# Optimization experiments

Hardware: AMD Instinct MI355X
Metric: run time of the kernel (lower is better)

Reference implementation:

```python
import jax, jax.numpy as jnp
import numpy as np

N_STATE = 64
N_LAYERS = 4
D_MODEL = 512
D_OUT = 256
BATCH = 16
SEQLEN = 2048


def setup_inputs() -> dict:
    key = jax.random.key(0)
    ks = jax.random.split(key, 16)
    H, N, nl = D_MODEL, N_STATE, N_LAYERS
    inp = {}
    inp["x"] = jax.random.normal(ks[0], (BATCH, SEQLEN, D_MODEL), dtype=jnp.float32)
    # encoder / decoder dense
    inp["enc_w"] = jax.random.normal(ks[1], (D_MODEL, D_MODEL), jnp.float32) / np.sqrt(D_MODEL)
    inp["enc_b"] = jnp.zeros((D_MODEL,), jnp.float32)
    inp["dec_w"] = jax.random.normal(ks[2], (D_MODEL, D_OUT), jnp.float32) / np.sqrt(D_MODEL)
    inp["dec_b"] = jnp.zeros((D_OUT,), jnp.float32)
    # per-layer LayerNorm
    inp["ln_scale"] = jnp.ones((nl, D_MODEL), jnp.float32)
    inp["ln_bias"] = jnp.zeros((nl, D_MODEL), jnp.float32)
    # per-layer S4 DPLR params (stored as real/imag float pairs)
    inp["lambda_re"] = -0.5 * jnp.ones((nl, H, N), jnp.float32)
    inp["lambda_im"] = jnp.broadcast_to(np.pi * jnp.arange(N, dtype=jnp.float32), (nl, H, N))
    inp["p_re"] = jax.random.normal(ks[3], (nl, H, N), jnp.float32) * 0.5
    inp["p_im"] = jax.random.normal(ks[4], (nl, H, N), jnp.float32) * 0.5
    inp["b_re"] = jax.random.normal(ks[5], (nl, H, N), jnp.float32) * 0.5
    inp["b_im"] = jax.random.normal(ks[6], (nl, H, N), jnp.float32) * 0.5
    inp["c_re"] = jax.random.normal(ks[7], (nl, H, N), jnp.float32) * 0.5
    inp["c_im"] = jax.random.normal(ks[8], (nl, H, N), jnp.float32) * 0.5
    inp["log_step"] = jax.random.uniform(ks[9], (nl, H), jnp.float32, minval=np.log(1e-3), maxval=np.log(1e-1))
    inp["d_param"] = jnp.ones((nl, H), jnp.float32)
    # per-layer output Dense
    inp["out_w"] = jax.random.normal(ks[10], (nl, D_MODEL, D_MODEL), jnp.float32) / np.sqrt(D_MODEL)
    inp["out_b"] = jnp.zeros((nl, D_MODEL), jnp.float32)
    return inp


def _layer_norm(x, scale, bias, eps=1e-6):
    mu = jnp.mean(x, axis=-1, keepdims=True)
    var = jnp.mean(jnp.square(x - mu), axis=-1, keepdims=True)
    return (x - mu) * jax.lax.rsqrt(var + eps) * scale + bias


def _kernel_dplr(Lam, P, B, C, step, L):
    # Lam,P,B,C: [H,N] complex64; step: [H] float32 -> K: [H,L] float32
    theta = (2.0 * np.pi / L) * jnp.arange(L, dtype=jnp.float32)
    Omega = jnp.exp(-1j * theta)                        # [L] roots of unity
    g = (2.0 / step)[:, None] * ((1.0 - Omega) / (1.0 + Omega))[None, :]  # [H,L]
    c = 2.0 / (1.0 + Omega)                             # [L]
    r = 1.0 / (g[:, :, None] - Lam[:, None, :])         # [H,L,N] resolvent (Cauchy)
    Cc, Pc = jnp.conj(C), jnp.conj(P)
    k00 = jnp.einsum("hn,hln->hl", Cc * B, r)
    k01 = jnp.einsum("hn,hln->hl", Cc * P, r)
    k10 = jnp.einsum("hn,hln->hl", Pc * B, r)
    k11 = jnp.einsum("hn,hln->hl", Pc * P, r)
    at_roots = c[None, :] * (k00 - k01 * (1.0 / (1.0 + k11)) * k10)  # [H,L]
    return jnp.fft.ifft(at_roots, n=L, axis=-1).real


def _s4_apply(u, Lam, P, B, C, step, D):
    # u: [Bt,L,H]; causal FFT convolution with kernel K[h,:] per channel
    L = u.shape[1]
    K = _kernel_dplr(Lam, P, B, C, step, L)             # [H,L]
    ud = jnp.fft.rfft(u, n=2 * L, axis=1)               # [Bt,L+1,H]
    Kd = jnp.fft.rfft(K, n=2 * L, axis=-1)              # [H,L+1]
    y = jnp.fft.irfft(ud * Kd.T[None], n=2 * L, axis=1)[:, :L]
    return y + D[None, None, :] * u


def reference(x, enc_w, enc_b, ln_scale, ln_bias, lambda_re, lambda_im,
              p_re, p_im, b_re, b_im, c_re, c_im, log_step, d_param,
              out_w, out_b, dec_w, dec_b):
    h = x @ enc_w + enc_b
    n_layers = ln_scale.shape[0]
    for i in range(n_layers):
        skip = h
        z = _layer_norm(h, ln_scale[i], ln_bias[i])
        Lam = lambda_re[i] + 1j * lambda_im[i]
        P = p_re[i] + 1j * p_im[i]
        B = b_re[i] + 1j * b_im[i]
        C = c_re[i] + 1j * c_im[i]
        z = _s4_apply(z, Lam, P, B, C, jnp.exp(log_step[i]), d_param[i])
        z = jax.nn.gelu(z)
        z = z @ out_w[i] + out_b[i]
        h = skip + z  # dropout=0.0 -> identity
    logits = h @ dec_w + dec_b
    return jax.nn.log_softmax(logits, axis=-1)
```

## Files before the change

kernel.cpp:

```cpp
#include <hip/hip_runtime.h>
#include <hip/hip_bf16.h>

#define NLAY 4
#define DH   512
#define NST  64
#define NB   16
#define SL   2048
#define NDO  256
#define BL   (NB*SL)
#define KDIM 512
#define TWOPI 6.283185307179586476925287

typedef unsigned short u16;
typedef __attribute__((ext_vector_type(8))) short  short8v;
typedef __attribute__((ext_vector_type(8))) unsigned short ushort8v;
typedef __attribute__((ext_vector_type(4))) float  f32x4;
typedef __attribute__((ext_vector_type(2))) unsigned int uint2v;

#define RCPF(x) __builtin_amdgcn_rcpf(x)

__device__ __forceinline__ float bf2f(u16 v){
  union { unsigned u; float f; } x; x.u = ((unsigned)v) << 16; return x.f;
}
__device__ __forceinline__ u16 f2bf(float f){
  union { float f; unsigned u; } x; x.f = f;
  unsigned u = x.u;
  unsigned r = u + 0x7fffu + ((u >> 16) & 1u);
  return (u16)(r >> 16);
}
__device__ __forceinline__ void cmulw(float& xr, float& xi, float wr, float wi){
  float tr = xr*wr - xi*wi;
  xi = fmaf(xr, wi, xi*wr);
  xr = tr;
}
__device__ __forceinline__ float gelu_fast(float v){
  const float c0 = 0.7978845608028654f;
  float u = c0 * fmaf(0.044715f, v*v*v, v);
  return v * RCPF(1.0f + __expf(-2.0f * u));
}
__device__ __forceinline__ void gload16(const void* g, void* l){
  __builtin_amdgcn_global_load_lds(
      (__attribute__((address_space(1))) void*)(g),
      (__attribute__((address_space(3))) void*)(l), 16, 0, 0);
}

__device__ __forceinline__ void twapply(float* re, float* im, float a){
  float ci, cr;
  __sincosf(a, &ci, &cr);
  float wr = cr, wi = ci;
#pragma unroll
  for (int k = 1; k < 16; k++){
    cmulw(re[k], im[k], wr, wi);
    const float nr = wr*cr - wi*ci;
    wi = fmaf(wr, ci, wi*cr);
    wr = nr;
  }
}

template<int SGN>
__device__ __forceinline__ void dft4w(float& r0, float& i0, float& r1, float& i1,
                                      float& r2, float& i2, float& r3, float& i3){
  const float t0r = r0 + r2, t0i = i0 + i2;
  const float t1r = r0 - r2, t1i = i0 - i2;
  const float t2r = r1 + r3, t2i = i1 + i3;
  const float t3r = r1 - r3, t3i = i1 - i3;
  r0 = t0r + t2r; i0 = t0i + t2i;
  r2 = t0r - t2r; i2 = t0i - t2i;
  if (SGN < 0){ r1 = t1r + t3i; i1 = t1i - t3r; r3 = t1r - t3i; i3 = t1i + t3r; }
  else        { r1 = t1r - t3i; i1 = t1i + t3r; r3 = t1r + t3i; i3 = t1i - t3r; }
}

template<int SGN>
__device__ __forceinline__ void dft16tail(float* re, float* im){
  const float C1 = 0.92387953251128675613f, S1_ = 0.38268343236508977172f;
  const float C2 = 0.70710678118654752440f;
  const float sg = (SGN < 0) ? -1.f : 1.f;
  cmulw(re[5],  im[5],   C1,  sg*S1_);
  cmulw(re[9],  im[9],   C2,  sg*C2);
  cmulw(re[13], im[13],  S1_, sg*C1);
  cmulw(re[6],  im[6],   C2,  sg*C2);
  cmulw(re[10], im[10],  0.f, sg*1.f);
  cmulw(re[14], im[14], -C2,  sg*C2);
  cmulw(re[7],  im[7],   S1_, sg*C1);
  cmulw(re[11], im[11], -C2,  sg*C2);
  cmulw(re[15], im[15], -C1,  sg*(-S1_));
#pragma unroll
  for (int c = 0; c < 4; c++)
    dft4w<SGN>(re[4*c], im[4*c], re[4*c+1], im[4*c+1], re[4*c+2], im[4*c+2], re[4*c+3], im[4*c+3]);
  float tr_, ti_;
#define SWP(A,B) tr_=re[A]; re[A]=re[B]; re[B]=tr_; ti_=im[A]; im[A]=im[B]; im[B]=ti_;
  SWP(1,4) SWP(2,8) SWP(3,12) SWP(6,9) SWP(7,13) SWP(11,14)
#undef SWP
}

template<int SGN>
__device__ __forceinline__ void dft16(float* re, float* im){
#pragma unroll
  for (int b = 0; b < 4; b++)
    dft4w<SGN>(re[b], im[b], re[4+b], im[4+b], re[8+b], im[8+b], re[12+b], im[12+b]);
  dft16tail<SGN>(re, im);
}

__device__ __forceinline__ void dft16fh(float* re, float* im){
#pragma unroll
  for (int b = 0; b < 4; b++){
    const float r0 = re[b], i0 = im[b], r1 = re[4+b], i1 = im[4+b];
    re[b]    = r0 + r1; im[b]    = i0 + i1;
    re[4+b]  = r0 + i1; im[4+b]  = i0 - r1;
    re[8+b]  = r0 - r1; im[8+b]  = i0 - i1;
    re[12+b] = r0 - i1; im[12+b] = i0 + r1;
  }
  dft16tail<-1>(re, im);
}

__device__ __forceinline__ int cxpad(int i){ return i + (i >> 4) + ((i >> 8) << 1); }
#define CXSZ 4384

__device__ __forceinline__ void fwd4096(float* re, float* im, float2* cx, int t){
  dft16fh(re, im);
  twapply(re, im, -(float)(TWOPI/4096.0) * (float)t);
#pragma unroll
  for (int k = 0; k < 16; k++) cx[cxpad(t + 256*k)] = make_float2(re[k], im[k]);
  __syncthreads();
  const int k1 = t >> 4, m2 = t & 15;
  const int b2 = k1*256 + m2;
#pragma unroll
  for (int j = 0; j < 16; j++){ float2 v = cx[cxpad(b2 + 16*j)]; re[j] = v.x; im[j] = v.y; }
  dft16<-1>(re, im);
  twapply(re, im, -(float)(TWOPI/256.0) * (float)m2);
#pragma unroll
  for (int k = 0; k < 16; k++) cx[cxpad(b2 + 16*k)] = make_float2(re[k], im[k]);
  __syncthreads();
#pragma unroll
  for (int j = 0; j < 16; j++){ float2 v = cx[cxpad(16*t + j)]; re[j] = v.x; im[j] = v.y; }
  dft16<-1>(re, im);
}

__device__ __forceinline__ void inv4096(float* re, float* im, float2* cx, int t){
  dft16<1>(re, im);
#pragma unroll
  for (int j = 0; j < 16; j++) cx[cxpad(16*t + j)] = make_float2(re[j], im[j]);
  __syncthreads();
  const int k1 = t >> 4, m2 = t & 15;
  const int b2 = k1*256 + m2;
#pragma unroll
  for (int k = 0; k < 16; k++){ float2 v = cx[cxpad(b2 + 16*k)]; re[k] = v.x; im[k] = v.y; }
  twapply(re, im, (float)(TWOPI/256.0) * (float)m2);
  dft16<1>(re, im);
#pragma unroll
  for (int j = 0; j < 16; j++) cx[cxpad(b2 + 16*j)] = make_float2(re[j], im[j]);
  __syncthreads();
#pragma unroll
  for (int k = 0; k < 16; k++){ float2 v = cx[cxpad(t + 256*k)]; re[k] = v.x; im[k] = v.y; }
  twapply(re, im, (float)(TWOPI/4096.0) * (float)t);
  dft16<1>(re, im);
}

__global__ __launch_bounds__(256) void prep_k(
  const float* __restrict__ lam_re, const float* __restrict__ lam_im,
  const float* __restrict__ p_re,  const float* __restrict__ p_im,
  const float* __restrict__ b_re,  const float* __restrict__ b_im,
  const float* __restrict__ c_re,  const float* __restrict__ c_im,
  float4* __restrict__ cwA, float4* __restrict__ cwB, float* __restrict__ cwS)
{
  const int i = blockIdx.x * 256 + threadIdx.x;
  const float lr = lam_re[i], li = lam_im[i];
  const float pr = p_re[i],  pi = p_im[i];
  const float br = b_re[i],  bi = b_im[i];
  const float cr = c_re[i],  ci = c_im[i];
  cwA[i] = make_float4(lr, li, cr*br + ci*bi, cr*bi - ci*br);
  cwB[i] = make_float4(cr*pr + ci*pi, cr*pi - ci*pr, pr*br + pi*bi, pr*bi - pi*br);
  cwS[i] = pr*pr + pi*pi;
}

__global__ __launch_bounds__(256) void cauchy_k(
    const float4* __restrict__ cwA, const float4* __restrict__ cwB,
    const float* __restrict__ cwS, const float* __restrict__ lstep,
    float2* __restrict__ Kd)
{
  const int t = threadIdx.x;
  const int h = blockIdx.y, lay = blockIdx.z;
  const int lb = blockIdx.x * 256 + t;
  const int wb = (lay*DH + h) * NST;
  const float tw0 = 2.0f * expf(-lstep[lay*DH + h]);

  float T0,T1, g0,g1;
  { float sn, cs;
    sincosf((float)(TWOPI/4096.0)*(float)(lb       ), &sn, &cs); T0 = sn*RCPF(cs); g0 = tw0*T0;
    sincosf((float)(TWOPI/4096.0)*(float)(lb + 1024), &sn, &cs); T1 = sn*RCPF(cs); g1 = tw0*T1;
  }

  float k00r0=0,k00i0=0,k01r0=0,k01i0=0,k10r0=0,k10i0=0,k11r0=0,k11i0=0;
  float k00r1=0,k00i1=0,k01r1=0,k01i1=0,k10r1=0,k10i1=0,k11r1=0,k11i1=0;

#pragma unroll 2
  for (int n = 0; n < NST; n++){
    const float4 A  = cwA[wb + n];
    const float4 Bv = cwB[wb + n];
    const float w11 = cwS[wb + n];
    const float nlr = -A.x;
    const float dr2 = A.x * A.x;
#define CSTEP(J) { \
    const float di = g##J - A.y; \
    const float sI = RCPF(fmaf(di, di, dr2)); \
    const float ivr = nlr * sI, ivi = -di * sI; \
    k00r##J = fmaf(A.z,  ivr, fmaf(-A.w,  ivi, k00r##J)); \
    k00i##J = fmaf(A.z,  ivi, fmaf( A.w,  ivr, k00i##J)); \
    k01r##J = fmaf(Bv.x, ivr, fmaf(-Bv.y, ivi, k01r##J)); \
    k01i##J = fmaf(Bv.x, ivi, fmaf( Bv.y, ivr, k01i##J)); \
    k10r##J = fmaf(Bv.z, ivr, fmaf(-Bv.w, ivi, k10r##J)); \
    k10i##J = fmaf(Bv.z, ivi, fmaf( Bv.w, ivr, k10i##J)); \
    k11r##J = fmaf(w11,  ivr, k11r##J); \
    k11i##J = fmaf(w11,  ivi, k11i##J); }
    CSTEP(0) CSTEP(1)
#undef CSTEP
  }

  float2* kp = Kd + (size_t)(lay*DH + h) * 4096;
#define COUT(J, LOFF) { \
    const float d1r = 1.f + k11r##J, d1i = k11i##J; \
    const float idn = RCPF(fmaf(d1r, d1r, d1i*d1i)); \
    const float wr = k01r##J*k10r##J - k01i##J*k10i##J; \
    const float wi = k01r##J*k10i##J + k01i##J*k10r##J; \
    const float vr = fmaf(wr, d1r,  wi*d1i) * idn; \
    const float vi = fmaf(wi, d1r, -wr*d1i) * idn; \
    const float sr = k00r##J - vr, si = k00i##J - vi; \
    kp[lb + LOFF] = make_float2(fmaf(-T##J, si, sr), fmaf(T##J, sr, si)); }
  COUT(0, 0) COUT(1, 1024)
#undef COUT
}

__global__ __launch_bounds__(256) void kdfft_k(float2* __restrict__ Kd){
  __shared__ float  ar[SL], ai[SL];
  __shared__ float2 cx[CXSZ];
  const int t = threadIdx.x;
  const size_t base = (size_t)blockIdx.x * 4096;
#pragma unroll
  for (int q = 0; q < 8; q++){
    const int l = t + 256*q;
    float2 v = Kd[base + l];
    const int brv = __brev((unsigned)l) >> 21;
    ar[brv] = v.x; ai[brv] = v.y;
  }
  __syncthreads();

  for (int s = 0; s < 11; s++){
    const int half = 1 << s;
    const float fac = (float)(TWOPI) / (float)(2 << s);
#pragma unroll
    for (int q = 0; q < 4; q++){
      const int v = t + 256*q;
      const int pos = v & (half - 1);
      const int i0 = ((v >> s) << (s+1)) + pos;
      const int i1 = i0 + half;
      const float ang = fac * (float)pos;
      const float wc = __cosf(ang), ws = __sinf(ang);
      const float xr = ar[i1], xi = ai[i1];
      const float tr = wc*xr - ws*xi, ti = fmaf(wc, xi, ws*xr);
      const float ur_ = ar[i0], ui_ = ai[i0];
      ar[i0] = ur_ + tr; ai[i0] = ui_ + ti;
      ar[i1] = ur_ - tr; ai[i1] = ui_ - ti;
    }
    __syncthreads();
  }

  float re[16], im[16];
#pragma unroll
  for (int j = 0; j < 16; j++){
    re[j] = (j < 8) ? ar[t + 256*j] * (1.0f/2048.f) : 0.f;
    im[j] = 0.f;
  }
  fwd4096(re, im, cx, t);
  float2* kp = Kd + base + 16*t;
#pragma unroll
  for (int k = 0; k < 16; k += 2)
    *(float4*)(kp + k) = make_float4(re[k], im[k], re[k+1], im[k+1]);
}

__global__ __launch_bounds__(256) void wconv_all_k(
    const float* __restrict__ enc_w, const float* __restrict__ out_w,
    const float* __restrict__ dec_w, u16* __restrict__ Wt)
{
  const int z = blockIdx.z;
  const float* src; u16* dst; int N;
  if (z == 0){ src = enc_w; dst = Wt; N = DH; }
  else if (z <= 4){ src = out_w + (size_t)(z-1)*KDIM*DH; dst = Wt + (size_t)z*262144; N = DH; }
  else { if (blockIdx.y >= 4) return; src = dec_w; dst = Wt + (size_t)5*262144; N = NDO; }
  __shared__ u16 tile[64][72];
  const int k0 = blockIdx.x * 64, n0 = blockIdx.y * 64;
  const int r = threadIdx.x >> 2, c4 = (threadIdx.x & 3) * 16;
  const float* s = src + (size_t)(k0 + r) * N + n0 + c4;
  float4 f0 = *(const float4*)s, f1 = *(const float4*)(s+4);
  float4 f2 = *(const float4*)(s+8), f3 = *(const float4*)(s+12);
  tile[c4+0][r]=f2bf(f0.x); tile[c4+1][r]=f2bf(f0.y); tile[c4+2][r]=f2bf(f0.z); tile[c4+3][r]=f2bf(f0.w);
  tile[c4+4][r]=f2bf(f1.x); tile[c4+5][r]=f2bf(f1.y); tile[c4+6][r]=f2bf(f1.z); tile[c4+7][r]=f2bf(f1.w);
  tile[c4+8][r]=f2bf(f2.x); tile[c4+9][r]=f2bf(f2.y); tile[c4+10][r]=f2bf(f2.z); tile[c4+11][r]=f2bf(f2.w);
  tile[c4+12][r]=f2bf(f3.x); tile[c4+13][r]=f2bf(f3.y); tile[c4+14][r]=f2bf(f3.z); tile[c4+15][r]=f2bf(f3.w);
  __syncthreads();
  u16* d = dst + (size_t)(n0 + r) * KDIM + k0 + c4;
  *(ushort8v*)d       = *(const ushort8v*)&tile[r][c4];
  *(ushort8v*)(d + 8) = *(const ushort8v*)&tile[r][c4 + 8];
}

#define LTILE 32
__device__ __forceinline__ int lnswz(int h){ return ((h >> 1) + (h >> 6)) & 3; }

__global__ __launch_bounds__(256) void lnt_k(const u16* __restrict__ hsrc,
    const float* __restrict__ gam, const float* __restrict__ bet,
    u16* __restrict__ zT){
  __shared__ u16 tile[DH][LTILE];
  __shared__ float smu[LTILE], srs[LTILE];
  const int t = threadIdx.x;
  const int b = blockIdx.y, l0 = blockIdx.x * LTILE;
  const int r = t >> 3, hb = (t & 7) * 64;
  const u16* p = hsrc + ((size_t)b * SL + l0 + r) * DH + hb;
  float s = 0.f, sq = 0.f;
#pragma unroll
  for (int j8 = 0; j8 < 8; j8++){
    ushort8v w = *(const ushort8v*)(p + j8*8);
    const int h0 = hb + j8*8;
#pragma unroll
    for (int d = 0; d < 8; d++){
      const float f = bf2f((u16)w[d]);
      s += f; sq = fmaf(f, f, sq);
      tile[h0+d][r ^ (lnswz(h0+d) << 3)] = (u16)w[d];
    }
  }
  s  += __shfl_xor(s, 1);  sq += __shfl_xor(sq, 1);
  s  += __shfl_xor(s, 2);  sq += __shfl_xor(sq, 2);
  s  += __shfl_xor(s, 4);  sq += __shfl_xor(sq, 4);
  if ((t & 7) == 0){
    const float mu = s * (1.0f/DH);
    smu[r] = mu;
    srs[r] = rsqrtf(sq * (1.0f/DH) - mu*mu + 1e-6f);
  }
  __syncthreads();

#pragma unroll
  for (int hh = 0; hh < 2; hh++){
    const int h = t + hh*256;
    const float g = gam[h], be = bet[h];
    const int sw = lnswz(h);
    u16* dst = zT + ((size_t)b * DH + h) * SL + l0;
#pragma unroll
    for (int og = 0; og < 4; og++){
      const int lg = og ^ sw;
      ushort8v v = *(const ushort8v*)&tile[h][og*8];
      const float4 m0 = *(const float4*)&smu[lg*8];
      const float4 m1 = *(const float4*)&smu[lg*8 + 4];
      const float4 r0 = *(const float4*)&srs[lg*8];
      const float4 r1 = *(const float4*)&srs[lg*8 + 4];
      ushort8v o;
      o[0] = f2bf(fmaf(bf2f((u16)v[0]) - m0.x, r0.x*g, be));
      o[1] = f2bf(fmaf(bf2f((u16)v[1]) - m0.y, r0.y*g, be));
      o[2] = f2bf(fmaf(bf2f((u16)v[2]) - m0.z, r0.z*g, be));
      o[3] = f2bf(fmaf(bf2f((u16)v[3]) - m0.w, r0.w*g, be));
      o[4] = f2bf(fmaf(bf2f((u16)v[4]) - m1.x, r1.x*g, be));
      o[5] = f2bf(fmaf(bf2f((u16)v[5]) - m1.y, r1.y*g, be));
      o[6] = f2bf(fmaf(bf2f((u16)v[6]) - m1.z, r1.z*g, be));
      o[7] = f2bf(fmaf(bf2f((u16)v[7]) - m1.w, r1.w*g, be));
      *(ushort8v*)(dst + lg*8) = o;
    }
  }
}

__global__ __launch_bounds__(256) void s4conv_k(
    const u16* __restrict__ zT, const float2* __restrict__ Kd,
    const float* __restrict__ dpar, u16* __restrict__ yT)
{
  __shared__ float2 cx[CXSZ];
  const int t = threadIdx.x;
  const int wg = blockIdx.x;
  const int h = wg & 511, bp = wg >> 9;
  const u16* r1 = zT + ((size_t)(2*bp) * DH + h) * SL;
  const u16* r2 = r1 + (size_t)DH * SL;
  float ur1[8], ur2[8];
  float re[16], im[16];
#pragma unroll
  for (int j = 0; j < 8; j++){
    ur1[j] = bf2f(r1[t + 256*j]);
    ur2[j] = bf2f(r2[t + 256*j]);
    re[j] = ur1[j]; im[j] = ur2[j];
  }
#pragma unroll
  for (int j = 8; j < 16; j++){ re[j] = 0.f; im[j] = 0.f; }

  fwd4096(re, im, cx, t);

  const float2* kp = Kd + (size_t)h * 4096 + 16*t;
#pragma unroll
  for (int k = 0; k < 16; k += 2){
    float4 w2 = *(const float4*)(kp + k);
    cmulw(re[k],   im[k],   w2.x, w2.y);
    cmulw(re[k+1], im[k+1], w2.z, w2.w);
  }

  inv4096(re, im, cx, t);

  const float Dv = dpar[h];
  u16* y1 = yT + ((size_t)(2*bp) * DH + h) * SL;
  u16* y2 = y1 + (size_t)DH * SL;
#pragma unroll
  for (int j = 0; j < 8; j++){
    float v1 = fmaf(re[j], (1.0f/4096.f), Dv * ur1[j]);
    float v2 = fmaf(im[j], (1.0f/4096.f), Dv * ur2[j]);
    y1[t + 256*j] = f2bf(gelu_fast(v1));
    y2[t + 256*j] = f2bf(gelu_fast(v2));
  }
}

__global__ __launch_bounds__(256) void gemm_at_k(
    const u16* __restrict__ A, const u16* __restrict__ Wt,
    const float* __restrict__ bias,
    const u16* __restrict__ resid, u16* __restrict__ Cout,
    int Mb, int N)
{
  __shared__ u16 As[4096];
  __shared__ u16 Bs[4096];
  const int t = threadIdx.x;
  const int n0 = blockIdx.x * 128, m0 = blockIdx.y * 128, bb = blockIdx.z;
  const int lane = t & 63, wv = t >> 6;
  const int wm = (wv >> 1) * 64, wn = (wv & 1) * 64;
  const int wbase = t & 192;
  f32x4 acc[4][4];
#pragma unroll
  for (int mi = 0; mi < 4; mi++)
#pragma unroll
    for (int ni = 0; ni < 4; ni++) acc[mi][ni] = {0.f, 0.f, 0.f, 0.f};

  int kA[2], mA[2];
#pragma unroll
  for (int i = 0; i < 2; i++){
    const int G = i*256 + t;
    const int s = G >> 3, r8 = G & 7;
    const int q = s & 7;
    const int kb = ((q & 3) << 1) | (q >> 2);
    kA[i] = kb*4 + (r8 >> 1);
    mA[i] = (s >> 3)*16 + (r8 & 1)*8;
  }
  const size_t Abase = (size_t)bb * DH * (size_t)Mb;
  const unsigned lds_as =
      (unsigned)(unsigned long long)(__attribute__((address_space(3))) u16*)As;

  for (int k0 = 0; k0 < KDIM; k0 += 32){
    __syncthreads();
#pragma unroll
    for (int i = 0; i < 2; i++)
      gload16(A + Abase + (size_t)(k0 + kA[i]) * Mb + m0 + mA[i],
              As + (size_t)(i*256 + wbase) * 8);
#pragma unroll
    for (int i = 0; i < 2; i++){
      const int G = i*256 + t;
      const int r = G >> 2;
      const int g = ((G & 3) ^ r ^ (r >> 2)) & 3;
      gload16(Wt + (size_t)(n0 + r) * KDIM + k0 + g*8,
              Bs + (size_t)(i*256 + wbase) * 8);
    }
    __syncthreads();

    uint2v ra[4], rb[4];
#pragma unroll
    for (int mi = 0; mi < 4; mi++){
      const unsigned b = lds_as + (unsigned)(((wm >> 4) + mi) * 1024 + lane * 8);
      asm volatile("ds_read_b64_tr_b16 %0, %1" : "=v"(ra[mi]) : "v"(b));
      asm volatile("ds_read_b64_tr_b16 %0, %1 offset:512" : "=v"(rb[mi]) : "v"(b));
    }
    asm volatile("s_waitcnt lgkmcnt(0)" ::: "memory");
    __builtin_amdgcn_sched_barrier(0);

    short8v af[4], bf[4];
#pragma unroll
    for (int mi = 0; mi < 4; mi++){
      union { uint2v u2[2]; short8v s8; } cvt;
      cvt.u2[0] = ra[mi]; cvt.u2[1] = rb[mi];
      af[mi] = cvt.s8;
    }
    const int fr = lane & 15, g4 = lane >> 4;
#pragma unroll
    for (int ni = 0; ni < 4; ni++){
      const int r = wn + ni*16 + fr;
      bf[ni] = *(const short8v*)&Bs[(size_t)((r<<2) | ((g4 ^ r ^ (r>>2)) & 3)) * 8];
    }
#pragma unroll
    for (int mi = 0; mi < 4; mi++)
#pragma unroll
      for (int ni = 0; ni < 4; ni++)
        acc[mi][ni] = __builtin_amdgcn_mfma_f32_16x16x32_bf16(af[mi], bf[ni], acc[mi][ni], 0, 0, 0);
  }

  const int fr = lane & 15;
  const int rq = (lane >> 4) * 4;
#pragma unroll
  for (int mi = 0; mi < 4; mi++){
#pragma unroll
    for (int ni = 0; ni < 4; ni++){
      const int gn = n0 + wn + ni*16 + fr;
      const float bs = bias[gn];
#pragma unroll
      for (int q = 0; q < 4; q++){
        const int gm = m0 + wm + mi*16 + rq + q;
        const size_t idx = ((size_t)bb * Mb + gm) * N + gn;
        Cout[idx] = f2bf(acc[mi][ni][q] + bs + bf2f(resid[idx]));
      }
    }
  }
}

__global__ __launch_bounds__(256) void gemm_enc_k(
    const float* __restrict__ Af, const u16* __restrict__ Wt,
    const float* __restrict__ bias, u16* __restrict__ Cout,
    int Mb, int N)
{
  __shared__ u16 As[4096];
  __shared__ u16 Bs[4096];
  const int t = threadIdx.x;
  const int n0 = blockIdx.x * 128, m0 = blockIdx.y * 128;
  const int lane = t & 63, wv = t >> 6;
  const int wm = (wv >> 1) * 64, wn = (wv & 1) * 64;
  const int wbase = t & 192;
  f32x4 acc[4][4];
#pragma unroll
  for (int mi = 0; mi < 4; mi++)
#pragma unroll
    for (int ni = 0; ni < 4; ni++) acc[mi][ni] = {0.f, 0.f, 0.f, 0.f};

  for (int k0 = 0; k0 < KDIM; k0 += 32){
    __syncthreads();
    {
      const int r = t >> 1, kh = (t & 1) << 4;
      const float* sf = Af + (size_t)(m0 + r) * KDIM + k0 + kh;
      float4 f0 = *(const float4*)sf,     f1 = *(const float4*)(sf + 4);
      float4 f2 = *(const float4*)(sf+8), f3 = *(const float4*)(sf + 12);
      ushort8v v0, v1;
      v0[0]=f2bf(f0.x); v0[1]=f2bf(f0.y); v0[2]=f2bf(f0.z); v0[3]=f2bf(f0.w);
      v0[4]=f2bf(f1.x); v0[5]=f2bf(f1.y); v0[6]=f2bf(f1.z); v0[7]=f2bf(f1.w);
      v1[0]=f2bf(f2.x); v1[1]=f2bf(f2.y); v1[2]=f2bf(f2.z); v1[3]=f2bf(f2.w);
      v1[4]=f2bf(f3.x); v1[5]=f2bf(f3.y); v1[6]=f2bf(f3.z); v1[7]=f2bf(f3.w);
      const int key = (r ^ (r >> 2)) & 3;
      *(ushort8v*)&As[(size_t)((r<<2) | ((kh>>3) ^ key))*8]       = v0;
      *(ushort8v*)&As[(size_t)((r<<2) | (((kh>>3)+1) ^ key))*8]   = v1;
    }
#pragma unroll
    for (int i = 0; i < 2; i++){
      const int G = i*256 + t;
      const int r = G >> 2;
      const int g = ((G & 3) ^ r ^ (r >> 2)) & 3;
      gload16(Wt + (size_t)(n0 + r) * KDIM + k0 + g*8,
              Bs + (size_t)(i*256 + wbase) * 8);
    }
    __syncthreads();

    const int fr = lane & 15, g4 = lane >> 4;
    short8v af[4], bf[4];
#pragma unroll
    for (int mi = 0; mi < 4; mi++){
      const int r = wm + mi*16 + fr;
      af[mi] = *(const short8v*)&As[(size_t)((r<<2) | ((g4 ^ r ^ (r>>2)) & 3)) * 8];
    }
#pragma unroll
    for (int ni = 0; ni < 4; ni++){
      const int r = wn + ni*16 + fr;
      bf[ni] = *(const short8v*)&Bs[(size_t)((r<<2) | ((g4 ^ r ^ (r>>2)) & 3)) * 8];
    }
#pragma unroll
    for (int mi = 0; mi < 4; mi++)
#pragma unroll
      for (int ni = 0; ni < 4; ni++)
        acc[mi][ni] = __builtin_amdgcn_mfma_f32_16x16x32_bf16(af[mi], bf[ni], acc[mi][ni], 0, 0, 0);
  }

  const int fr = lane & 15;
  const int rq = (lane >> 4) * 4;
#pragma unroll
  for (int mi = 0; mi < 4; mi++){
#pragma unroll
    for (int ni = 0; ni < 4; ni++){
      const int gn = n0 + wn + ni*16 + fr;
      const float bs = bias[gn];
#pragma unroll
      for (int q = 0; q < 4; q++){
        const int gm = m0 + wm + mi*16 + rq + q;
        Cout[(size_t)gm * N + gn] = f2bf(acc[mi][ni][q] + bs);
      }
    }
  }
}

__global__ __launch_bounds__(256) void gemm_dec_k(
    const u16* __restrict__ A, const u16* __restrict__ Wt,
    const float* __restrict__ bias, float* __restrict__ Out)
{
  __shared__ u16 As[4096];
  __shared__ u16 Bs[8192];
  const int t = threadIdx.x;
  const int m0 = blockIdx.x * 128;
  const int lane = t & 63, wv = t >> 6;
  const int wm = wv * 32;
  const int wbase = t & 192;
  f32x4 acc[2][16];
#pragma unroll
  for (int mi = 0; mi < 2; mi++)
#pragma unroll
    for (int ni = 0; ni < 16; ni++) acc[mi][ni] = {0.f, 0.f, 0.f, 0.f};

  for (int k0 = 0; k0 < KDIM; k0 += 32){
    __syncthreads();
#pragma unroll
    for (int i = 0; i < 2; i++){
      const int G = i*256 + t;
      const int r = G >> 2;
      const int g = ((G & 3) ^ r ^ (r >> 2)) & 3;
      gload16(A + (size_t)(m0 + r) * KDIM + k0 + g*8,
              As + (size_t)(i*256 + wbase) * 8);
    }
#pragma unroll
    for (int i = 0; i < 4; i++){
      const int G = i*256 + t;
      const int r = G >> 2;
      const int g = ((G & 3) ^ r ^ (r >> 2)) & 3;
      gload16(Wt + (size_t)r * KDIM + k0 + g*8,
              Bs + (size_t)(i*256 + wbase) * 8);
    }
    __syncthreads();

    const int fr = lane & 15, g4 = lane >> 4;
    short8v af[2], bf[16];
#pragma unroll
    for (int mi = 0; mi < 2; mi++){
      const int r = wm + mi*16 + fr;
      af[mi] = *(const short8v*)&As[(size_t)((r<<2) | ((g4 ^ r ^ (r>>2)) & 3)) * 8];
    }
#pragma unroll
    for (int ni = 0; ni < 16; ni++){
      const int r = ni*16 + fr;
      bf[ni] = *(const short8v*)&Bs[(size_t)((r<<2) | ((g4 ^ r ^ (r>>2)) & 3)) * 8];
    }
#pragma unroll
    for (int mi = 0; mi < 2; mi++)
#pragma unroll
      for (int ni = 0; ni < 16; ni++)
        acc[mi][ni] = __builtin_amdgcn_mfma_f32_16x16x32_bf16(af[mi], bf[ni], acc[mi][ni], 0, 0, 0);
  }

  const int fr = lane & 15, g4 = lane >> 4;
  float bssv[16];
#pragma unroll
  for (int ni = 0; ni < 16; ni++) bssv[ni] = bias[ni*16 + fr];

#pragma unroll
  for (int mi = 0; mi < 2; mi++){
#pragma unroll
    for (int q = 0; q < 4; q++){
      float v[16];
      float mx = -3.4e38f;
#pragma unroll
      for (int ni = 0; ni < 16; ni++){
        v[ni] = acc[mi][ni][q] + bssv[ni];
        mx = fmaxf(mx, v[ni]);
      }
      mx = fmaxf(mx, __shfl_xor(mx, 1));
      mx = fmaxf(mx, __shfl_xor(mx, 2));
      mx = fmaxf(mx, __shfl_xor(mx, 4));
      mx = fmaxf(mx, __shfl_xor(mx, 8));
      float e = 0.f;
#pragma unroll
      for (int ni = 0; ni < 16; ni++) e += __expf(v[ni] - mx);
      e += __shfl_xor(e, 1);
      e += __shfl_xor(e, 2);
      e += __shfl_xor(e, 4);
      e += __shfl_xor(e, 8);
      const float lse = mx + __logf(e);
      const int gm = m0 + wm + mi*16 + g4*4 + q;
      float* po = Out + (size_t)gm * NDO + fr;
#pragma unroll
      for (int ni = 0; ni < 16; ni++) po[ni*16] = v[ni] - lse;
    }
  }
}

extern "C" void kernel_launch(void* const* d_in, const int* in_sizes, int n_in,
                              void* d_out, int out_size, void* d_ws, size_t ws_size,
                              hipStream_t stream)
{
  (void)in_sizes; (void)n_in; (void)out_size; (void)ws_size;
  const float* x      = (const float*)d_in[0];
  const float* enc_w  = (const float*)d_in[1];
  const float* enc_b  = (const float*)d_in[2];
  const float* dec_w  = (const float*)d_in[3];
  const float* dec_b  = (const float*)d_in[4];
  const float* ln_s   = (const float*)d_in[5];
  const float* ln_b   = (const float*)d_in[6];
  const float* lam_re = (const float*)d_in[7];
  const float* lam_im = (const float*)d_in[8];
  const float* p_re   = (const float*)d_in[9];
  const float* p_im   = (const float*)d_in[10];
  const float* b_re   = (const float*)d_in[11];
  const float* b_im   = (const float*)d_in[12];
  const float* c_re   = (const float*)d_in[13];
  const float* c_im   = (const float*)d_in[14];
  const float* lstep  = (const float*)d_in[15];
  const float* d_par  = (const float*)d_in[16];
  const float* out_w  = (const float*)d_in[17];
  const float* out_b  = (const float*)d_in[18];

  char* ws = (char*)d_ws;
  u16*    hbuf = (u16*)(ws);
  u16*    zT   = (u16*)  (ws + (size_t)67108864 + 33554432);
  u16*    yT   = (u16*)  (ws + (size_t)67108864 + 2*33554432);
  float2* Kd   = (float2*)(ws + (size_t)67108864 + 3*33554432);
  u16*    Wt   = (u16*)  (ws + (size_t)67108864 + 3*33554432 + 67108864);
  u16*    WtOut = Wt + 262144;
  u16*    WtDec = Wt + 262144*5;
  float*  outp = (float*)d_out;

  float4* cwA = (float4*)d_out;
  float4* cwB = cwA + 131072;
  float*  cwS = (float*)(cwB + 131072);

  prep_k<<<dim3(NLAY*DH*NST/256), 256, 0, stream>>>(lam_re, lam_im, p_re, p_im,
                                                    b_re, b_im, c_re, c_im, cwA, cwB, cwS);
  wconv_all_k<<<dim3(8, 8, 6), 256, 0, stream>>>(enc_w, out_w, dec_w, Wt);
  cauchy_k<<<dim3(4, DH, NLAY), 256, 0, stream>>>(cwA, cwB, cwS, lstep, Kd);
  kdfft_k<<<dim3(NLAY*DH), 256, 0, stream>>>(Kd);
  gemm_enc_k<<<dim3(DH/128, BL/128, 1), 256, 0, stream>>>(
      x, Wt, enc_b, hbuf, BL, DH);
  for (int i = 0; i < NLAY; i++){
    lnt_k<<<dim3(SL/LTILE, NB), 256, 0, stream>>>(hbuf, ln_s + i*DH, ln_b + i*DH, zT);
    s4conv_k<<<dim3((NB/2)*DH), 256, 0, stream>>>(
        zT, Kd + (size_t)i*DH*4096, d_par + i*DH, yT);
    gemm_at_k<<<dim3(DH/128, SL/128, NB), 256, 0, stream>>>(
        yT, WtOut + (size_t)i*262144, out_b + i*DH, hbuf, hbuf, SL, DH);
  }
  gemm_dec_k<<<dim3(BL/128), 256, 0, stream>>>(hbuf, WtDec, dec_b, outp);
}
```

Before: 700.6 us.

## Pair Cauchy poles to halve reciprocals in DPLR kernel evaluation

```diff
diff --git a/kernel.cpp b/kernel.cpp
--- a/kernel.cpp
+++ b/kernel.cpp
@@ -156,32 +156,52 @@
   dft16<1>(re, im);
 }
 
-__global__ __launch_bounds__(256) void prep_k(
+__global__ __launch_bounds__(256) void prep2_k(
   const float* __restrict__ lam_re, const float* __restrict__ lam_im,
   const float* __restrict__ p_re,  const float* __restrict__ p_im,
   const float* __restrict__ b_re,  const float* __restrict__ b_im,
   const float* __restrict__ c_re,  const float* __restrict__ c_im,
-  float4* __restrict__ cwA, float4* __restrict__ cwB, float* __restrict__ cwS)
+  float4* __restrict__ Wp)
 {
-  const int i = blockIdx.x * 256 + threadIdx.x;
-  const float lr = lam_re[i], li = lam_im[i];
-  const float pr = p_re[i],  pi = p_im[i];
-  const float br = b_re[i],  bi = b_im[i];
-  const float cr = c_re[i],  ci = c_im[i];
-  cwA[i] = make_float4(lr, li, cr*br + ci*bi, cr*bi - ci*br);
-  cwB[i] = make_float4(cr*pr + ci*pi, cr*pi - ci*pr, pr*br + pi*bi, pr*bi - pi*br);
-  cwS[i] = pr*pr + pi*pi;
+  const int q = blockIdx.x * 256 + threadIdx.x;
+  const int e = q * 2;
+  const float lar = lam_re[e],   lai = lam_im[e];
+  const float lbr = lam_re[e+1], lbi = lam_im[e+1];
+  const float par_ = p_re[e],   pai = p_im[e];
+  const float pbr  = p_re[e+1], pbi = p_im[e+1];
+  const float bar_ = b_re[e],   bai = b_im[e];
+  const float bbr  = b_re[e+1], bbi = b_im[e+1];
+  const float car_ = c_re[e],   cai = c_im[e];
+  const float cbr  = c_re[e+1], cbi = c_im[e+1];
+  const float a00r = car_*bar_ + cai*bai, a00i = car_*bai - cai*bar_;
+  const float b00r = cbr*bbr + cbi*bbi,   b00i = cbr*bbi - cbi*bbr;
+  const float a01r = car_*par_ + cai*pai, a01i = car_*pai - cai*par_;
+  const float b01r = cbr*pbr + cbi*pbi,   b01i = cbr*pbi - cbi*pbr;
+  const float a10r = par_*bar_ + pai*bai, a10i = par_*bai - pai*bar_;
+  const float b10r = pbr*bbr + pbi*bbi,   b10i = pbr*bbi - pbi*bbr;
+  const float a11 = par_*par_ + pai*pai,  b11 = pbr*pbr + pbi*pbi;
+  Wp[(size_t)q*5 + 0] = make_float4(lar + lbr, lai + lbi,
+                                    lar*lbr - lai*lbi, lar*lbi + lai*lbr);
+#define UV(ar,ai,br,bi,SLOT) { \
+  const float Vr = -(((ar)*lbr - (ai)*lbi) + ((br)*lar - (bi)*lai)); \
+  const float Vi = -(((ar)*lbi + (ai)*lbr) + ((br)*lai + (bi)*lar)); \
+  Wp[(size_t)q*5 + SLOT] = make_float4((ar)+(br), (ai)+(bi), Vr, Vi); }
+  UV(a00r,a00i,b00r,b00i,1)
+  UV(a01r,a01i,b01r,b01i,2)
+  UV(a10r,a10i,b10r,b10i,3)
+#undef UV
+  Wp[(size_t)q*5 + 4] = make_float4(a11 + b11, 0.f,
+                                    -(a11*lbr + b11*lar), -(a11*lbi + b11*lai));
 }
 
 __global__ __launch_bounds__(256) void cauchy_k(
-    const float4* __restrict__ cwA, const float4* __restrict__ cwB,
-    const float* __restrict__ cwS, const float* __restrict__ lstep,
+    const float4* __restrict__ Wp, const float* __restrict__ lstep,
     float2* __restrict__ Kd)
 {
   const int t = threadIdx.x;
   const int h = blockIdx.y, lay = blockIdx.z;
   const int lb = blockIdx.x * 256 + t;
-  const int wb = (lay*DH + h) * NST;
+  const float4* W = Wp + (size_t)(lay*DH + h) * 32 * 5;
   const float tw0 = 2.0f * expf(-lstep[lay*DH + h]);
 
   float T0,T1, g0,g1;
@@ -189,31 +209,37 @@
     sincosf((float)(TWOPI/4096.0)*(float)(lb       ), &sn, &cs); T0 = sn*RCPF(cs); g0 = tw0*T0;
     sincosf((float)(TWOPI/4096.0)*(float)(lb + 1024), &sn, &cs); T1 = sn*RCPF(cs); g1 = tw0*T1;
   }
+  const float g0_2 = g0*g0, g1_2 = g1*g1;
 
   float k00r0=0,k00i0=0,k01r0=0,k01i0=0,k10r0=0,k10i0=0,k11r0=0,k11i0=0;
   float k00r1=0,k00i1=0,k01r1=0,k01i1=0,k10r1=0,k10i1=0,k11r1=0,k11i1=0;
 
 #pragma unroll 2
-  for (int n = 0; n < NST; n++){
-    const float4 A  = cwA[wb + n];
-    const float4 Bv = cwB[wb + n];
-    const float w11 = cwS[wb + n];
-    const float nlr = -A.x;
-    const float dr2 = A.x * A.x;
-#define CSTEP(J) { \
-    const float di = g##J - A.y; \
-    const float sI = RCPF(fmaf(di, di, dr2)); \
-    const float ivr = nlr * sI, ivi = -di * sI; \
-    k00r##J = fmaf(A.z,  ivr, fmaf(-A.w,  ivi, k00r##J)); \
-    k00i##J = fmaf(A.z,  ivi, fmaf( A.w,  ivr, k00i##J)); \
-    k01r##J = fmaf(Bv.x, ivr, fmaf(-Bv.y, ivi, k01r##J)); \
-    k01i##J = fmaf(Bv.x, ivi, fmaf( Bv.y, ivr, k01i##J)); \
-    k10r##J = fmaf(Bv.z, ivr, fmaf(-Bv.w, ivi, k10r##J)); \
-    k10i##J = fmaf(Bv.z, ivi, fmaf( Bv.w, ivr, k10i##J)); \
-    k11r##J = fmaf(w11,  ivr, k11r##J); \
-    k11i##J = fmaf(w11,  ivi, k11i##J); }
-    CSTEP(0) CSTEP(1)
-#undef CSTEP
+  for (int p = 0; p < 32; p++){
+    const float4 P0 = W[p*5 + 0];
+    const float4 P1 = W[p*5 + 1];
+    const float4 P2 = W[p*5 + 2];
+    const float4 P3 = W[p*5 + 3];
+    const float4 P4 = W[p*5 + 4];
+#define PSTEP(J) { \
+    const float Dr = fmaf(g##J, P0.y, P0.z - g##J##_2); \
+    const float Di = fmaf(-g##J, P0.x, P0.w); \
+    const float sI = RCPF(fmaf(Dr, Dr, Di*Di)); \
+    const float Er = Dr * sI, Ei = -(Di * sI); \
+    { const float Nr = fmaf(-P1.y, g##J, P1.z), Ni = fmaf(P1.x, g##J, P1.w); \
+      k00r##J = fmaf(Nr, Er, fmaf(-Ni, Ei, k00r##J)); \
+      k00i##J = fmaf(Nr, Ei, fmaf( Ni, Er, k00i##J)); } \
+    { const float Nr = fmaf(-P2.y, g##J, P2.z), Ni = fmaf(P2.x, g##J, P2.w); \
+      k01r##J = fmaf(Nr, Er, fmaf(-Ni, Ei, k01r##J)); \
+      k01i##J = fmaf(Nr, Ei, fmaf( Ni, Er, k01i##J)); } \
+    { const float Nr = fmaf(-P3.y, g##J, P3.z), Ni = fmaf(P3.x, g##J, P3.w); \
+      k10r##J = fmaf(Nr, Er, fmaf(-Ni, Ei, k10r##J)); \
+      k10i##J = fmaf(Nr, Ei, fmaf( Ni, Er, k10i##J)); } \
+    { const float Nr = P4.z, Ni = fmaf(P4.x, g##J, P4.w); \
+      k11r##J = fmaf(Nr, Er, fmaf(-Ni, Ei, k11r##J)); \
+      k11i##J = fmaf(Nr, Ei, fmaf( Ni, Er, k11i##J)); } }
+    PSTEP(0) PSTEP(1)
+#undef PSTEP
   }
 
   float2* kp = Kd + (size_t)(lay*DH + h) * 4096;
@@ -713,14 +739,12 @@
   u16*    WtDec = Wt + 262144*5;
   float*  outp = (float*)d_out;
 
-  float4* cwA = (float4*)d_out;
-  float4* cwB = cwA + 131072;
-  float*  cwS = (float*)(cwB + 131072);
-
-  prep_k<<<dim3(NLAY*DH*NST/256), 256, 0, stream>>>(lam_re, lam_im, p_re, p_im,
-                                                    b_re, b_im, c_re, c_im, cwA, cwB, cwS);
+  float4* Wp = (float4*)d_out;
+
+  prep2_k<<<dim3(NLAY*DH*32/256), 256, 0, stream>>>(lam_re, lam_im, p_re, p_im,
+                                                    b_re, b_im, c_re, c_im, Wp);
   wconv_all_k<<<dim3(8, 8, 6), 256, 0, stream>>>(enc_w, out_w, dec_w, Wt);
-  cauchy_k<<<dim3(4, DH, NLAY), 256, 0, stream>>>(cwA, cwB, cwS, lstep, Kd);
+  cauchy_k<<<dim3(4, DH, NLAY), 256, 0, stream>>>(Wp, lstep, Kd);
   kdfft_k<<<dim3(NLAY*DH), 256, 0, stream>>>(Kd);
   gemm_enc_k<<<dim3(DH/128, BL/128, 1), 256, 0, stream>>>(
       x, Wt, enc_b, hbuf, BL, DH);
```

Measured after the change: 704.1 us. No clear change (+0.5%).
